# Optimization experiments

Hardware: AMD Instinct MI355X
Metric: run time of the kernel (lower is better)

## Reference

```python
import jax, jax.numpy as jnp
import numpy as np

B, N_UNITS, SEQ, H = 4, 1024, 2048, 8
D_HEAD = N_UNITS // H
SCALE = 1.0 / D_HEAD ** 0.5


def setup_inputs() -> dict:
    key = jax.random.key(0)
    k1, k2, k3 = jax.random.split(key, 3)
    x = jax.random.normal(k1, (B, N_UNITS, SEQ), dtype=jnp.float32)
    # conv1x1 weights, bias=False; scaled like typical init
    W_qkv = jax.random.normal(k2, (3 * N_UNITS, N_UNITS), dtype=jnp.float32) * (1.0 / N_UNITS ** 0.5)
    W_out = jax.random.normal(k3, (N_UNITS, N_UNITS), dtype=jnp.float32) * (1.0 / N_UNITS ** 0.5)
    return {"x": x, "W_qkv": W_qkv, "W_out": W_out}


def reference(x, W_qkv, W_out):
    # x: (B, n_units, S). Conv1x1 == per-position linear along channel dim.
    qkv = jnp.einsum('oc,bcs->bos', W_qkv, x)          # (B, 3*n_units, S)
    Q, K, V = jnp.split(qkv, 3, axis=1)                # each (B, n_units, S)
    # torch.chunk along channels into h heads == reshape (B, h, d_head, S)
    Q = Q.reshape(B, H, D_HEAD, SEQ)
    K = K.reshape(B, H, D_HEAD, SEQ)
    V = V.reshape(B, H, D_HEAD, SEQ)
    # scores: Q^T K * scale  (NO softmax in original module; mask unused)
    A = jnp.einsum('bhdq,bhdk->bhqk', Q, K) * SCALE    # (B, h, S, S)
    # aggregation: sum_k A[q,k] * V[d,k]  (original does broadcast mul+sum)
    C = jnp.einsum('bhqk,bhdk->bhdq', A, V)            # (B, h, d_head, S)
    C = C.reshape(B, N_UNITS, SEQ)
    out = jnp.einsum('oc,bcs->bos', W_out, C)          # (B, n_units, S)
    return out
```

## Files before the change

kernel.cpp:

```cpp
#include <hip/hip_runtime.h>
#include <hip/hip_bf16.h>
#include <stdint.h>

using bf16 = __hip_bfloat16;

typedef __bf16 bf16x8 __attribute__((ext_vector_type(8)));
typedef float  f32x4  __attribute__((ext_vector_type(4)));

constexpr int Bc = 4, Hh = 8, Dh = 128, S = 2048, Cn = 1024, O3 = 3072;
constexpr float SCALE = 0.08838834764831845f;

#define GLDS16(gp, lp)                                               \
  __builtin_amdgcn_global_load_lds(                                  \
      (const __attribute__((address_space(1))) void*)(gp),           \
      (__attribute__((address_space(3))) void*)(lp), 16, 0, 0)

#define WAITVM(N) asm volatile("s_waitcnt vmcnt(" #N ")" ::: "memory")
#define BAR()                                  \
  do {                                         \
    asm volatile("" ::: "memory");             \
    __builtin_amdgcn_s_barrier();              \
    asm volatile("" ::: "memory");             \
  } while (0)

__device__ __forceinline__ void gemm_bt_core(
    const bf16* __restrict__ Abase, int lda,
    const bf16* __restrict__ Bbase, int ldb,
    int kIters, f32x4 (&acc)[4][4])
{
  alignas(16) __shared__ bf16 As[128 * 32];
  alignas(16) __shared__ bf16 Bs[128 * 32];
  const int t    = threadIdx.x;
  const int lane = t & 63;
  const int quad = lane >> 4, r16 = lane & 15;
  const int wave = t >> 6;
  const int wm = (wave & 1) * 64, wn = (wave >> 1) * 64;
  const int lrow = lane >> 2;
  const int lk   = (lane & 3) * 8;

  const long aOff0 = (long)(wave * 32 + lrow) * lda + lk;
  const long aOff1 = aOff0 + 16l * lda;
  const long bOff0 = (long)(wave * 32 + lrow) * ldb + lk;
  const long bOff1 = bOff0 + 16l * ldb;
  bf16* aL0 = &As[(wave * 32) * 32];
  bf16* aL1 = &As[(wave * 32 + 16) * 32];
  bf16* bL0 = &Bs[(wave * 32) * 32];
  bf16* bL1 = &Bs[(wave * 32 + 16) * 32];

#pragma unroll
  for (int i = 0; i < 4; i++)
#pragma unroll
    for (int j = 0; j < 4; j++) acc[i][j] = {0.f, 0.f, 0.f, 0.f};

  for (int ks = 0; ks < kIters; ++ks) {
    const int k0 = ks * 32;
    __syncthreads();
    GLDS16(Abase + k0 + aOff0, aL0);
    GLDS16(Abase + k0 + aOff1, aL1);
    GLDS16(Bbase + k0 + bOff0, bL0);
    GLDS16(Bbase + k0 + bOff1, bL1);
    __syncthreads();
    bf16x8 af[4], bfr[4];
#pragma unroll
    for (int i = 0; i < 4; i++)
      af[i] = *(const bf16x8*)&As[(wm + i * 16 + r16) * 32 + quad * 8];
#pragma unroll
    for (int j = 0; j < 4; j++)
      bfr[j] = *(const bf16x8*)&Bs[(wn + j * 16 + r16) * 32 + quad * 8];
#pragma unroll
    for (int i = 0; i < 4; i++)
#pragma unroll
      for (int j = 0; j < 4; j++)
        acc[i][j] = __builtin_amdgcn_mfma_f32_16x16x32_bf16(af[i], bfr[j], acc[i][j], 0, 0, 0);
  }
}

__device__ __forceinline__ void store_bf16_tile(
    f32x4 (&acc)[4][4], bf16* __restrict__ Cp, int ldc)
{
  const int t = threadIdx.x;
  const int lane = t & 63;
  const int quad = lane >> 4, r16 = lane & 15;
  const int wave = t >> 6;
  const int wm = (wave & 1) * 64, wn = (wave >> 1) * 64;
#pragma unroll
  for (int i = 0; i < 4; i++)
#pragma unroll
    for (int j = 0; j < 4; j++)
#pragma unroll
      for (int r = 0; r < 4; r++) {
        const int row = wm + i * 16 + quad * 4 + r;
        const int col = wn + j * 16 + r16;
        Cp[(long)row * ldc + col] = __float2bfloat16(acc[i][j][r]);
      }
}

__device__ __forceinline__ void store_f32_tile(
    f32x4 (&acc)[4][4], float* __restrict__ Cp, int ldc)
{
  const int t = threadIdx.x;
  const int lane = t & 63;
  const int quad = lane >> 4, r16 = lane & 15;
  const int wave = t >> 6;
  const int wm = (wave & 1) * 64, wn = (wave >> 1) * 64;
#pragma unroll
  for (int i = 0; i < 4; i++)
#pragma unroll
    for (int j = 0; j < 4; j++)
#pragma unroll
      for (int r = 0; r < 4; r++) {
        const int row = wm + i * 16 + quad * 4 + r;
        const int col = wn + j * 16 + r16;
        Cp[(long)row * ldc + col] = acc[i][j][r];
      }
}


__device__ __forceinline__ void kv_body(
    const bf16* __restrict__ WkvB, const bf16* __restrict__ xT,
    bf16* __restrict__ KV, bf16* sm, int orig)
{
  constexpr int NT = Cn / 32;
  const int mt = orig >> 6;
  const int nt = ((orig & 7) << 3) | ((orig >> 3) & 7);
  const int m0 = mt * 256;

  const int tid  = threadIdx.x;
  const int lane = tid & 63;
  const int w    = tid >> 6;
  const int quad = lane >> 4, r16 = lane & 15;
  const int wm = (w >> 1) * 64;
  const int wn = (w & 1) * 64;

  const int srow = w * 16 + (lane >> 2);
  const int cx   = (lane & 3) ^ ((lane >> 3) & 3);
  const bf16* Ag = WkvB + (long)(m0 + srow) * Cn + cx * 8;
  const bf16* Bg = xT + (long)((long)nt * 128 + srow) * Cn + cx * 8;
  const int ldsW = w * 512;

#define KV_STAGE(base, tt)                                                \
  do {                                                                    \
    const int k0_ = (tt) * 32;                                            \
    GLDS16(Ag + k0_,             (base) + ldsW);                          \
    GLDS16(Ag + 128l * Cn + k0_, (base) + 4096 + ldsW);                   \
    GLDS16(Bg + k0_,             (base) + 8192 + ldsW);                   \
  } while (0)

  const int sc8 = (quad ^ ((r16 >> 1) & 3)) * 8;

  f32x4 acc[4][4];
#pragma unroll
  for (int m = 0; m < 4; m++)
#pragma unroll
    for (int n = 0; n < 4; n++) acc[m][n] = {0.f, 0.f, 0.f, 0.f};

  bf16* bufc = sm;
  bf16* bufn = sm + 12288;
  bf16* bufs = sm + 24576;

  KV_STAGE(bufc, 0); KV_STAGE(bufn, 1);
  WAITVM(3);
  BAR();

  bf16x8 af0[2], af1[2], bfr0[4];
#pragma unroll
  for (int n = 0; n < 4; n++)
    bfr0[n] = *(const bf16x8*)&bufc[8192 + (wn + n * 16 + r16) * 32 + sc8];
#pragma unroll
  for (int m = 0; m < 2; m++)
    af0[m] = *(const bf16x8*)&bufc[(wm + m * 16 + r16) * 32 + sc8];

#pragma unroll 3
  for (int tt = 0; tt < NT; ++tt) {
    BAR();
    if (tt + 2 < NT) KV_STAGE(bufs, tt + 2);
#pragma unroll
    for (int m = 0; m < 2; m++)
      af1[m] = *(const bf16x8*)&bufc[(wm + (m + 2) * 16 + r16) * 32 + sc8];
    __builtin_amdgcn_s_setprio(1);
#pragma unroll
    for (int m = 0; m < 2; m++)
#pragma unroll
      for (int n = 0; n < 4; n++)
        acc[m][n] = __builtin_amdgcn_mfma_f32_16x16x32_bf16(af0[m], bfr0[n], acc[m][n], 0, 0, 0);
    __builtin_amdgcn_s_setprio(0);

    if (tt < NT - 2)       { WAITVM(3); }
    else if (tt == NT - 2) { WAITVM(0); }
    BAR();

    __builtin_amdgcn_s_setprio(1);
#pragma unroll
    for (int m = 0; m < 2; m++)
#pragma unroll
      for (int n = 0; n < 4; n++)
        acc[m + 2][n] = __builtin_amdgcn_mfma_f32_16x16x32_bf16(af1[m], bfr0[n], acc[m + 2][n], 0, 0, 0);
    __builtin_amdgcn_s_setprio(0);

    if (tt + 1 < NT) {
#pragma unroll
      for (int n = 0; n < 4; n++)
        bfr0[n] = *(const bf16x8*)&bufn[8192 + (wn + n * 16 + r16) * 32 + sc8];
#pragma unroll
      for (int m = 0; m < 2; m++)
        af0[m] = *(const bf16x8*)&bufn[(wm + m * 16 + r16) * 32 + sc8];
    }
    bf16* t_ = bufc; bufc = bufn; bufn = bufs; bufs = t_;
  }

  const int b = nt >> 4, scol = (nt & 15) * 128;
  bf16* Cp = KV + (long)b * 2048 * S + (long)m0 * S + scol;
#pragma unroll
  for (int m = 0; m < 4; m++)
#pragma unroll
    for (int n = 0; n < 4; n++)
#pragma unroll
      for (int r = 0; r < 4; r++) {
        const int row = wm + m * 16 + quad * 4 + r;
        const int col = wn + n * 16 + r16;
        Cp[(long)row * S + col] = __float2bfloat16(acc[m][n][r]);
      }
#undef KV_STAGE
}

__device__ __forceinline__ void qt_body(
    const bf16* __restrict__ xT, const bf16* __restrict__ WqB,
    bf16* __restrict__ QT, bf16* sm, int orig)
{
  constexpr int NT = Cn / 32;
  const int b  = orig >> 6;
  const int mt = (orig >> 2) & 15;
  const int nt = orig & 3;
  const int m0 = mt * 128, n0 = nt * 256;

  const int tid  = threadIdx.x;
  const int lane = tid & 63;
  const int w    = tid >> 6;
  const int quad = lane >> 4, r16 = lane & 15;
  const int wm = (w >> 2) * 64;
  const int wn = (w & 3) * 64;

  const int srow = w * 16 + (lane >> 2);
  const int cx   = (lane & 3) ^ ((lane >> 3) & 3);
  const bf16* Ag = xT + (long)b * S * Cn + (long)(m0 + srow) * Cn + cx * 8;
  const bf16* Bg = WqB + (long)(n0 + srow) * Cn + cx * 8;
  const int ldsW = w * 512;

#define QT_STAGE(base, tt)                                                \
  do {                                                                    \
    const int k0_ = (tt) * 32;                                            \
    GLDS16(Ag + k0_,             (base) + ldsW);                          \
    GLDS16(Bg + k0_,             (base) + 4096 + ldsW);                   \
    GLDS16(Bg + 128l * Cn + k0_, (base) + 8192 + ldsW);                   \
  } while (0)

  const int sc8 = (quad ^ ((r16 >> 1) & 3)) * 8;

  f32x4 acc[4][4];
#pragma unroll
  for (int m = 0; m < 4; m++)
#pragma unroll
    for (int n = 0; n < 4; n++) acc[m][n] = {0.f, 0.f, 0.f, 0.f};

  bf16* bufc = sm;
  bf16* bufn = sm + 12288;
  bf16* bufs = sm + 24576;

  QT_STAGE(bufc, 0); QT_STAGE(bufn, 1);
  WAITVM(3);
  BAR();

  bf16x8 af0[2], af1[2], bfr0[4];
#pragma unroll
  for (int n = 0; n < 4; n++)
    bfr0[n] = *(const bf16x8*)&bufc[4096 + (wn + n * 16 + r16) * 32 + sc8];
#pragma unroll
  for (int m = 0; m < 2; m++)
    af0[m] = *(const bf16x8*)&bufc[(wm + m * 16 + r16) * 32 + sc8];

#pragma unroll 3
  for (int tt = 0; tt < NT; ++tt) {
    BAR();
    if (tt + 2 < NT) QT_STAGE(bufs, tt + 2);
#pragma unroll
    for (int m = 0; m < 2; m++)
      af1[m] = *(const bf16x8*)&bufc[(wm + (m + 2) * 16 + r16) * 32 + sc8];
    __builtin_amdgcn_s_setprio(1);
#pragma unroll
    for (int m = 0; m < 2; m++)
#pragma unroll
      for (int n = 0; n < 4; n++)
        acc[m][n] = __builtin_amdgcn_mfma_f32_16x16x32_bf16(af0[m], bfr0[n], acc[m][n], 0, 0, 0);
    __builtin_amdgcn_s_setprio(0);

    if (tt < NT - 2)       { WAITVM(3); }
    else if (tt == NT - 2) { WAITVM(0); }
    BAR();

    __builtin_amdgcn_s_setprio(1);
#pragma unroll
    for (int m = 0; m < 2; m++)
#pragma unroll
      for (int n = 0; n < 4; n++)
        acc[m + 2][n] = __builtin_amdgcn_mfma_f32_16x16x32_bf16(af1[m], bfr0[n], acc[m + 2][n], 0, 0, 0);
    __builtin_amdgcn_s_setprio(0);

    if (tt + 1 < NT) {
#pragma unroll
      for (int n = 0; n < 4; n++)
        bfr0[n] = *(const bf16x8*)&bufn[4096 + (wn + n * 16 + r16) * 32 + sc8];
#pragma unroll
      for (int m = 0; m < 2; m++)
        af0[m] = *(const bf16x8*)&bufn[(wm + m * 16 + r16) * 32 + sc8];
    }
    bf16* t_ = bufc; bufc = bufn; bufn = bufs; bufs = t_;
  }

  bf16* Cp = QT + (long)b * S * Cn + (long)m0 * Cn + n0;
#pragma unroll
  for (int m = 0; m < 4; m++)
#pragma unroll
    for (int n = 0; n < 4; n++)
#pragma unroll
      for (int r = 0; r < 4; r++) {
        const int row = wm + m * 16 + quad * 4 + r;
        const int col = wn + n * 16 + r16;
        Cp[(long)row * Cn + col] = __float2bfloat16(acc[m][n][r]);
      }
#undef QT_STAGE
}

__global__ __launch_bounds__(512, 4) void k_kvqt8(
    const bf16* __restrict__ WkvB, const bf16* __restrict__ xT,
    bf16* __restrict__ KV, const bf16* __restrict__ WqB, bf16* __restrict__ QT)
{
  alignas(16) __shared__ bf16 smem[3 * 12288];
  const int bid = blockIdx.x;
  if (bid < 512) kv_body(WkvB, xT, KV, smem, bid);
  else           qt_body(xT, WqB, QT, smem, bid - 512);
}

__global__ __launch_bounds__(512, 4) void k_gemm_out8(
    const bf16* __restrict__ W2, const bf16* __restrict__ QT, float* __restrict__ out)
{
  constexpr int NT = Cn / 32;
  alignas(16) __shared__ bf16 smem[3 * 12288];

  const int orig = blockIdx.x;
  const int swz  = (orig & 7) * 32 + (orig >> 3);
  const int b  = swz >> 6;
  const int mt = (swz >> 3) & 7;
  const int nt = swz & 7;
  const int m0 = mt * 128, n0 = nt * 256;

  const int tid  = threadIdx.x;
  const int lane = tid & 63;
  const int w    = tid >> 6;
  const int quad = lane >> 4, r16 = lane & 15;
  const int wm = (w >> 2) * 64;
  const int wn = (w & 3) * 64;

  const int srow = w * 16 + (lane >> 2);
  const int cx   = (lane & 3) ^ ((lane >> 3) & 3);
  const bf16* Ag = W2 + (long)b * Cn * Cn + (long)(m0 + srow) * Cn + cx * 8;
  const bf16* Bg = QT + (long)b * S * Cn + (long)(n0 + srow) * Cn + cx * 8;
  const int ldsW = w * 512;

#define OUT_STAGE(base, tt)                                               \
  do {                                                                    \
    const int k0_ = (tt) * 32;                                            \
    GLDS16(Ag + k0_,             (base) + ldsW);                          \
    GLDS16(Bg + k0_,             (base) + 4096 + ldsW);                   \
    GLDS16(Bg + 128l * Cn + k0_, (base) + 8192 + ldsW);                   \
  } while (0)

  const int sc8 = (quad ^ ((r16 >> 1) & 3)) * 8;

  f32x4 acc[4][4];
#pragma unroll
  for (int m = 0; m < 4; m++)
#pragma unroll
    for (int n = 0; n < 4; n++) acc[m][n] = {0.f, 0.f, 0.f, 0.f};

  bf16* bufc = smem;
  bf16* bufn = smem + 12288;
  bf16* bufs = smem + 24576;

  OUT_STAGE(bufc, 0); OUT_STAGE(bufn, 1);
  WAITVM(3);
  BAR();

  bf16x8 af0[2], af1[2], bfr0[4];
#pragma unroll
  for (int n = 0; n < 4; n++)
    bfr0[n] = *(const bf16x8*)&bufc[4096 + (wn + n * 16 + r16) * 32 + sc8];
#pragma unroll
  for (int m = 0; m < 2; m++)
    af0[m] = *(const bf16x8*)&bufc[(wm + m * 16 + r16) * 32 + sc8];

#pragma unroll 3
  for (int tt = 0; tt < NT; ++tt) {
    BAR();
    if (tt + 2 < NT) OUT_STAGE(bufs, tt + 2);
#pragma unroll
    for (int m = 0; m < 2; m++)
      af1[m] = *(const bf16x8*)&bufc[(wm + (m + 2) * 16 + r16) * 32 + sc8];
    __builtin_amdgcn_s_setprio(1);
#pragma unroll
    for (int m = 0; m < 2; m++)
#pragma unroll
      for (int n = 0; n < 4; n++)
        acc[m][n] = __builtin_amdgcn_mfma_f32_16x16x32_bf16(af0[m], bfr0[n], acc[m][n], 0, 0, 0);
    __builtin_amdgcn_s_setprio(0);

    if (tt < NT - 2)       { WAITVM(3); }
    else if (tt == NT - 2) { WAITVM(0); }
    BAR();

    __builtin_amdgcn_s_setprio(1);
#pragma unroll
    for (int m = 0; m < 2; m++)
#pragma unroll
      for (int n = 0; n < 4; n++)
        acc[m + 2][n] = __builtin_amdgcn_mfma_f32_16x16x32_bf16(af1[m], bfr0[n], acc[m + 2][n], 0, 0, 0);
    __builtin_amdgcn_s_setprio(0);

    if (tt + 1 < NT) {
#pragma unroll
      for (int n = 0; n < 4; n++)
        bfr0[n] = *(const bf16x8*)&bufn[4096 + (wn + n * 16 + r16) * 32 + sc8];
#pragma unroll
      for (int m = 0; m < 2; m++)
        af0[m] = *(const bf16x8*)&bufn[(wm + m * 16 + r16) * 32 + sc8];
    }
    bf16* t_ = bufc; bufc = bufn; bufn = bufs; bufs = t_;
  }

  float* Cp = out + (long)b * Cn * S + (long)m0 * S + n0;
#pragma unroll
  for (int m = 0; m < 4; m++)
#pragma unroll
    for (int n = 0; n < 4; n++)
#pragma unroll
      for (int r = 0; r < 4; r++) {
        const int row = wm + m * 16 + quad * 4 + r;
        const int col = wn + n * 16 + r16;
        Cp[(long)row * S + col] = acc[m][n][r];
      }
#undef OUT_STAGE
}

__global__ __launch_bounds__(256) void k_prep(
    const float* __restrict__ x, bf16* __restrict__ xT,
    const float* __restrict__ Wqkv, const float* __restrict__ Wout,
    bf16* __restrict__ WqkvB, bf16* __restrict__ WoutB)
{
  __shared__ bf16 tile[32][33];
  if (blockIdx.z < 4) {
    const float* ip = x + (long)blockIdx.z * 1024 * 2048;
    bf16* op = xT + (long)blockIdx.z * 2048 * 1024;
    const int c0 = blockIdx.x * 32, r0 = blockIdx.y * 32;
    const int tx = threadIdx.x & 31, ty = threadIdx.x >> 5;
#pragma unroll
    for (int i = 0; i < 32; i += 8)
      tile[ty + i][tx] = __float2bfloat16(ip[(long)(r0 + ty + i) * 2048 + c0 + tx]);
    __syncthreads();
#pragma unroll
    for (int i = 0; i < 32; i += 8)
      op[(long)(c0 + ty + i) * 1024 + r0 + tx] = tile[tx][ty + i];
  } else {
    const long blk = (long)blockIdx.x + (long)blockIdx.y * 64;
#pragma unroll
    for (int i = 0; i < 2; i++) {
      const long v = blk * 512 + i * 256 + threadIdx.x;
      const bool isQ = v < 786432;
      const float4 f = isQ ? ((const float4*)Wqkv)[v] : ((const float4*)Wout)[v - 786432];
      bf16 tmp[4];
      tmp[0] = __float2bfloat16(f.x);
      tmp[1] = __float2bfloat16(f.y);
      tmp[2] = __float2bfloat16(f.z);
      tmp[3] = __float2bfloat16(f.w);
      ushort4 u = *(ushort4*)tmp;
      if (isQ) ((ushort4*)WqkvB)[v] = u;
      else     ((ushort4*)WoutB)[v - 786432] = u;
    }
  }
}

__global__ __launch_bounds__(256) void k_gemm_mt(
    const bf16* __restrict__ KV, float* __restrict__ MTpart)
{
  const int chunk = blockIdx.x;
  const int z = blockIdx.y;
  const int b = z >> 3, h = z & 7;
  const bf16* base = KV + (long)b * 2048 * S;
  const bf16* A  = base + (long)(h * Dh) * S + chunk * 256;
  const bf16* Bp = base + (long)(1024 + h * Dh) * S + chunk * 256;
  f32x4 acc[4][4];
  gemm_bt_core(A, S, Bp, S, 8, acc);
  store_f32_tile(acc, MTpart + ((long)chunk * 32 + z) * (Dh * Dh), Dh);
}

__global__ __launch_bounds__(256) void k_reduce_mt(
    const float* __restrict__ MTpart, bf16* __restrict__ MbT)
{
  const long i = (long)blockIdx.x * 256 + threadIdx.x;
  float s = 0.f;
#pragma unroll
  for (int c = 0; c < 8; c++) s += MTpart[(long)c * 32 * Dh * Dh + i];
  MbT[i] = __float2bfloat16(s * SCALE);
}

__global__ __launch_bounds__(256) void k_gemm_w2(
    const bf16* __restrict__ WoutB, const bf16* __restrict__ MbT, bf16* __restrict__ W2)
{
  const int m0 = blockIdx.x * 128;
  const int h = blockIdx.y, b = blockIdx.z;
  const int z = b * 8 + h;
  f32x4 acc[4][4];
  gemm_bt_core(WoutB + (long)m0 * Cn + h * Dh, Cn,
               MbT + (long)z * Dh * Dh, Dh, 4, acc);
  store_bf16_tile(acc, W2 + (long)b * Cn * Cn + (long)m0 * Cn + h * Dh, Cn);
}

extern "C" void kernel_launch(void* const* d_in, const int* in_sizes, int n_in,
                              void* d_out, int out_size, void* d_ws, size_t ws_size,
                              hipStream_t stream)
{
  const float* x    = (const float*)d_in[0];
  const float* Wqkv = (const float*)d_in[1];
  const float* Wout = (const float*)d_in[2];
  float* out = (float*)d_out;

  char* ws = (char*)d_ws;
  bf16*  KV     = (bf16*)ws;
  bf16*  xT     = (bf16*)(ws + 33554432);
  bf16*  QT     = (bf16*)(ws + 50331648);
  bf16*  WqkvB  = (bf16*)(ws + 67108864);
  bf16*  WoutB  = (bf16*)(ws + 73400320);
  bf16*  MbT    = (bf16*)(ws + 75497472);
  bf16*  W2     = (bf16*)(ws + 76546048);
  bf16*  WkvB   = WqkvB + (long)Cn * Cn;
  float* MTpart = out;

  k_prep<<<dim3(64, 32, 5), 256, 0, stream>>>(x, xT, Wqkv, Wout, WqkvB, WoutB);
  k_kvqt8<<<dim3(768), 512, 0, stream>>>(WkvB, xT, KV, WqkvB, QT);
  k_gemm_mt<<<dim3(8, 32), 256, 0, stream>>>(KV, MTpart);
  k_reduce_mt<<<dim3(2048), 256, 0, stream>>>(MTpart, MbT);
  k_gemm_w2<<<dim3(8, 8, 4), 256, 0, stream>>>(WoutB, MbT, W2);
  k_gemm_out8<<<dim3(256), 512, 0, stream>>>(W2, QT, out);
}
```

Before: 196.6 us.

## Split fused KV/QT GEMM and enlarge KV tiles to 256x256 with 4-stage pipeline

Result: no change. 194.9 us (-0.9%).

```diff
diff --git a/kernel.cpp b/kernel.cpp
--- a/kernel.cpp
+++ b/kernel.cpp
@@ -115,103 +115,114 @@
       }
 }
 
-
-__device__ __forceinline__ void kv_body(
-    const bf16* __restrict__ WkvB, const bf16* __restrict__ xT,
-    bf16* __restrict__ KV, bf16* sm, int orig)
+__global__ __launch_bounds__(512, 2) void k_gemm_kv8(
+    const bf16* __restrict__ WkvB, const bf16* __restrict__ xT, bf16* __restrict__ KV)
 {
   constexpr int NT = Cn / 32;
-  const int mt = orig >> 6;
-  const int nt = ((orig & 7) << 3) | ((orig >> 3) & 7);
+  alignas(16) __shared__ bf16 smem[4 * 16384];
+
+  const int orig = blockIdx.x;
+  const int mt = orig >> 5;
+  const int nt = ((orig & 7) << 2) | ((orig >> 3) & 3);
   const int m0 = mt * 256;
 
   const int tid  = threadIdx.x;
   const int lane = tid & 63;
   const int w    = tid >> 6;
   const int quad = lane >> 4, r16 = lane & 15;
-  const int wm = (w >> 1) * 64;
-  const int wn = (w & 1) * 64;
+  const int wm = (w >> 2) * 128;
+  const int wn = (w & 3) * 64;
 
   const int srow = w * 16 + (lane >> 2);
   const int cx   = (lane & 3) ^ ((lane >> 3) & 3);
   const bf16* Ag = WkvB + (long)(m0 + srow) * Cn + cx * 8;
-  const bf16* Bg = xT + (long)((long)nt * 128 + srow) * Cn + cx * 8;
+  const bf16* Bg = xT + (long)((long)nt * 256 + srow) * Cn + cx * 8;
   const int ldsW = w * 512;
 
-#define KV_STAGE(base, tt)                                                \
+#define KV8_STAGE_A(tt)                                                   \
   do {                                                                    \
-    const int k0_ = (tt) * 32;                                            \
-    GLDS16(Ag + k0_,             (base) + ldsW);                          \
-    GLDS16(Ag + 128l * Cn + k0_, (base) + 4096 + ldsW);                   \
-    GLDS16(Bg + k0_,             (base) + 8192 + ldsW);                   \
+    const int k0_ = (tt) * 32, bb_ = ((tt) & 3) * 16384;                  \
+    GLDS16(Ag + k0_,             &smem[bb_ + ldsW]);                      \
+    GLDS16(Ag + 128l * Cn + k0_, &smem[bb_ + 4096 + ldsW]);               \
   } while (0)
+#define KV8_STAGE_B(tt)                                                   \
+  do {                                                                    \
+    const int k0_ = (tt) * 32, bb_ = ((tt) & 3) * 16384;                  \
+    GLDS16(Bg + k0_,             &smem[bb_ + 8192 + ldsW]);               \
+    GLDS16(Bg + 128l * Cn + k0_, &smem[bb_ + 8192 + 4096 + ldsW]);        \
+  } while (0)
 
   const int sc8 = (quad ^ ((r16 >> 1) & 3)) * 8;
 
-  f32x4 acc[4][4];
-#pragma unroll
-  for (int m = 0; m < 4; m++)
+  f32x4 acc[8][4];
+#pragma unroll
+  for (int m = 0; m < 8; m++)
 #pragma unroll
     for (int n = 0; n < 4; n++) acc[m][n] = {0.f, 0.f, 0.f, 0.f};
 
-  bf16* bufc = sm;
-  bf16* bufn = sm + 12288;
-  bf16* bufs = sm + 24576;
-
-  KV_STAGE(bufc, 0); KV_STAGE(bufn, 1);
-  WAITVM(3);
+  KV8_STAGE_A(0); KV8_STAGE_B(0);
+  KV8_STAGE_A(1); KV8_STAGE_B(1);
+  KV8_STAGE_A(2); KV8_STAGE_B(2);
+  WAITVM(8);
   BAR();
 
-  bf16x8 af0[2], af1[2], bfr0[4];
-#pragma unroll
-  for (int n = 0; n < 4; n++)
-    bfr0[n] = *(const bf16x8*)&bufc[8192 + (wn + n * 16 + r16) * 32 + sc8];
-#pragma unroll
-  for (int m = 0; m < 2; m++)
-    af0[m] = *(const bf16x8*)&bufc[(wm + m * 16 + r16) * 32 + sc8];
-
-#pragma unroll 3
+  bf16x8 af0[4], bfr0[4], af1[4];
+  {
+    const bf16* Ab = &smem[0];
+    const bf16* Bb = Ab + 8192;
+#pragma unroll
+    for (int n = 0; n < 4; n++)
+      bfr0[n] = *(const bf16x8*)&Bb[(wn + n * 16 + r16) * 32 + sc8];
+#pragma unroll
+    for (int m = 0; m < 4; m++)
+      af0[m] = *(const bf16x8*)&Ab[(wm + m * 16 + r16) * 32 + sc8];
+  }
+
+#pragma unroll 4
   for (int tt = 0; tt < NT; ++tt) {
+    const bf16* Ab = &smem[(tt & 3) * 16384];
+
     BAR();
-    if (tt + 2 < NT) KV_STAGE(bufs, tt + 2);
-#pragma unroll
-    for (int m = 0; m < 2; m++)
-      af1[m] = *(const bf16x8*)&bufc[(wm + (m + 2) * 16 + r16) * 32 + sc8];
+    if (tt + 3 < NT) { KV8_STAGE_A(tt + 3); KV8_STAGE_B(tt + 3); }
+#pragma unroll
+    for (int m = 0; m < 4; m++)
+      af1[m] = *(const bf16x8*)&Ab[(wm + (m + 4) * 16 + r16) * 32 + sc8];
     __builtin_amdgcn_s_setprio(1);
 #pragma unroll
-    for (int m = 0; m < 2; m++)
+    for (int m = 0; m < 4; m++)
 #pragma unroll
       for (int n = 0; n < 4; n++)
         acc[m][n] = __builtin_amdgcn_mfma_f32_16x16x32_bf16(af0[m], bfr0[n], acc[m][n], 0, 0, 0);
     __builtin_amdgcn_s_setprio(0);
 
-    if (tt < NT - 2)       { WAITVM(3); }
+    if (tt <= NT - 4)      { WAITVM(8); }
+    else if (tt == NT - 3) { WAITVM(4); }
     else if (tt == NT - 2) { WAITVM(0); }
     BAR();
 
     __builtin_amdgcn_s_setprio(1);
 #pragma unroll
-    for (int m = 0; m < 2; m++)
-#pragma unroll
-      for (int n = 0; n < 4; n++)
-        acc[m + 2][n] = __builtin_amdgcn_mfma_f32_16x16x32_bf16(af1[m], bfr0[n], acc[m + 2][n], 0, 0, 0);
+    for (int m = 0; m < 4; m++)
+#pragma unroll
+      for (int n = 0; n < 4; n++)
+        acc[m + 4][n] = __builtin_amdgcn_mfma_f32_16x16x32_bf16(af1[m], bfr0[n], acc[m + 4][n], 0, 0, 0);
     __builtin_amdgcn_s_setprio(0);
 
     if (tt + 1 < NT) {
-#pragma unroll
-      for (int n = 0; n < 4; n++)
-        bfr0[n] = *(const bf16x8*)&bufn[8192 + (wn + n * 16 + r16) * 32 + sc8];
-#pragma unroll
-      for (int m = 0; m < 2; m++)
-        af0[m] = *(const bf16x8*)&bufn[(wm + m * 16 + r16) * 32 + sc8];
+      const bf16* Ab2 = &smem[((tt + 1) & 3) * 16384];
+      const bf16* Bb2 = Ab2 + 8192;
+#pragma unroll
+      for (int n = 0; n < 4; n++)
+        bfr0[n] = *(const bf16x8*)&Bb2[(wn + n * 16 + r16) * 32 + sc8];
+#pragma unroll
+      for (int m = 0; m < 4; m++)
+        af0[m] = *(const bf16x8*)&Ab2[(wm + m * 16 + r16) * 32 + sc8];
     }
-    bf16* t_ = bufc; bufc = bufn; bufn = bufs; bufs = t_;
   }
 
-  const int b = nt >> 4, scol = (nt & 15) * 128;
-  bf16* Cp = KV + (long)b * 2048 * S + (long)m0 * S + scol;
-#pragma unroll
-  for (int m = 0; m < 4; m++)
+  bf16* Cp = KV + (long)(nt >> 3) * 2048 * S + (long)m0 * S + (nt & 7) * 256;
+#pragma unroll
+  for (int m = 0; m < 8; m++)
 #pragma unroll
     for (int n = 0; n < 4; n++)
 #pragma unroll
@@ -220,14 +231,17 @@
         const int col = wn + n * 16 + r16;
         Cp[(long)row * S + col] = __float2bfloat16(acc[m][n][r]);
       }
-#undef KV_STAGE
-}
-
-__device__ __forceinline__ void qt_body(
-    const bf16* __restrict__ xT, const bf16* __restrict__ WqB,
-    bf16* __restrict__ QT, bf16* sm, int orig)
+#undef KV8_STAGE_A
+#undef KV8_STAGE_B
+}
+
+__global__ __launch_bounds__(512, 4) void k_gemm_qt8(
+    const bf16* __restrict__ xT, const bf16* __restrict__ WqB, bf16* __restrict__ QT)
 {
   constexpr int NT = Cn / 32;
+  alignas(16) __shared__ bf16 smem[3 * 12288];
+
+  const int orig = blockIdx.x;
   const int b  = orig >> 6;
   const int mt = (orig >> 2) & 15;
   const int nt = orig & 3;
@@ -262,9 +276,9 @@
 #pragma unroll
     for (int n = 0; n < 4; n++) acc[m][n] = {0.f, 0.f, 0.f, 0.f};
 
-  bf16* bufc = sm;
-  bf16* bufn = sm + 12288;
-  bf16* bufs = sm + 24576;
+  bf16* bufc = smem;
+  bf16* bufn = smem + 12288;
+  bf16* bufs = smem + 24576;
 
   QT_STAGE(bufc, 0); QT_STAGE(bufn, 1);
   WAITVM(3);
@@ -328,16 +342,6 @@
         Cp[(long)row * Cn + col] = __float2bfloat16(acc[m][n][r]);
       }
 #undef QT_STAGE
-}
-
-__global__ __launch_bounds__(512, 4) void k_kvqt8(
-    const bf16* __restrict__ WkvB, const bf16* __restrict__ xT,
-    bf16* __restrict__ KV, const bf16* __restrict__ WqB, bf16* __restrict__ QT)
-{
-  alignas(16) __shared__ bf16 smem[3 * 12288];
-  const int bid = blockIdx.x;
-  if (bid < 512) kv_body(WkvB, xT, KV, smem, bid);
-  else           qt_body(xT, WqB, QT, smem, bid - 512);
 }
 
 __global__ __launch_bounds__(512, 4) void k_gemm_out8(
@@ -544,7 +548,8 @@
   float* MTpart = out;
 
   k_prep<<<dim3(64, 32, 5), 256, 0, stream>>>(x, xT, Wqkv, Wout, WqkvB, WoutB);
-  k_kvqt8<<<dim3(768), 512, 0, stream>>>(WkvB, xT, KV, WqkvB, QT);
+  k_gemm_kv8<<<dim3(256), 512, 0, stream>>>(WkvB, xT, KV);
+  k_gemm_qt8<<<dim3(256), 512, 0, stream>>>(xT, WqkvB, QT);
   k_gemm_mt<<<dim3(8, 32), 256, 0, stream>>>(KV, MTpart);
   k_reduce_mt<<<dim3(2048), 256, 0, stream>>>(MTpart, MbT);
   k_gemm_w2<<<dim3(8, 8, 4), 256, 0, stream>>>(WoutB, MbT, W2);
```
